# Kernel optimization log

Hardware: AMD Instinct MI355X
Metric: run time of the kernel (lower is better)

The kernel has to match this reference:

```python
import jax, jax.numpy as jnp
import numpy as np

T = 20000          # document length in tokens
EMBED_DIM = 300    # GloVe 840B.300d
STATE_DIM = 400    # 2 * lstm_dim (bidirectional)
HIDDEN = 150       # Scorer hidden_dim default
MAX_N = 10         # span widths 1..10
G_DIM = 2 * STATE_DIM + EMBED_DIM  # 1100


def _mlp3(x, W1, b1, W2, b2, W3, b3):
    # Scorer: Linear -> ReLU -> Linear -> ReLU -> Linear(->1)
    h = jax.nn.relu(x @ W1 + b1)
    h = jax.nn.relu(h @ W2 + b2)
    return h @ W3 + b3


def _span_features(embeds, states, attn_logits):
    """Vectorized SpanEncoder: for every window of width n in 1..MAX_N,
    softmax the per-token attention logits within the window, attention-pool
    the word embeddings, and concat [state_start, state_end, pooled].
    Returns g of shape [sum_n (T-n+1), G_DIM]."""
    gs = []
    for n in range(1, MAX_N + 1):
        S = T - n + 1  # number of width-n spans
        # [n, S] windowed logits and [n, S, E] windowed embeds via shifted slices
        a = jnp.stack([attn_logits[j:j + S] for j in range(n)], axis=0)
        w = jax.nn.softmax(a, axis=0)  # softmax within each span (dim=0 in torch)
        we = jnp.stack([embeds[j:j + S] for j in range(n)], axis=0)
        pooled = jnp.einsum('ns,nse->se', w, we)  # [S, E]
        g = jnp.concatenate([states[:S], states[n - 1:n - 1 + S], pooled], axis=-1)
        gs.append(g)
    return jnp.concatenate(gs, axis=0)


def setup_inputs() -> dict:
    key = jax.random.key(0)
    ks = jax.random.split(key, 16)
    sc = 0.05
    return {
        'embeds': jax.random.normal(ks[0], (T, EMBED_DIM), jnp.float32),
        'states': jax.random.normal(ks[1], (T, STATE_DIM), jnp.float32),
        'attn_W1': jax.random.normal(ks[2], (STATE_DIM, HIDDEN), jnp.float32) * sc,
        'attn_b1': jnp.zeros((HIDDEN,), jnp.float32),
        'attn_W2': jax.random.normal(ks[3], (HIDDEN, HIDDEN), jnp.float32) * sc,
        'attn_b2': jnp.zeros((HIDDEN,), jnp.float32),
        'attn_W3': jax.random.normal(ks[4], (HIDDEN, 1), jnp.float32) * sc,
        'attn_b3': jnp.zeros((1,), jnp.float32),
        'sc_W1': jax.random.normal(ks[5], (G_DIM, HIDDEN), jnp.float32) * sc,
        'sc_b1': jnp.zeros((HIDDEN,), jnp.float32),
        'sc_W2': jax.random.normal(ks[6], (HIDDEN, HIDDEN), jnp.float32) * sc,
        'sc_b2': jnp.zeros((HIDDEN,), jnp.float32),
        'sc_W3': jax.random.normal(ks[7], (HIDDEN, 1), jnp.float32) * sc,
        'sc_b3': jnp.zeros((1,), jnp.float32),
    }


def reference(embeds, states, attn_W1, attn_b1, attn_W2, attn_b2, attn_W3, attn_b3,
              sc_W1, sc_b1, sc_W2, sc_b2, sc_W3, sc_b3):
    # SpanAttention: per-token scalar attention logit from the BiLSTM state
    attn_logits = _mlp3(states, attn_W1, attn_b1, attn_W2, attn_b2, attn_W3, attn_b3)[:, 0]
    # SpanEncoder: ragged windowed attention pooling + boundary-state concat
    g = _span_features(embeds, states, attn_logits)  # [10T-45, 1100]
    # SpanScorer: MLP score per span
    scores = _mlp3(g, sc_W1, sc_b1, sc_W2, sc_b2, sc_W3, sc_b3)[:, 0]
    return scores
```

## Files before the change

kernel.cpp:

```cpp
#include <hip/hip_runtime.h>
#include <hip/hip_bf16.h>
#include <math.h>

#define T_LEN 20000
#define HID 150

typedef __attribute__((ext_vector_type(8))) __bf16 bf16x8;
typedef __attribute__((ext_vector_type(4))) float f32x4;

__device__ __forceinline__ short f2bf(float f) {
    unsigned u = __float_as_uint(f);
    u = (u + 0x7fff + ((u >> 16) & 1)) >> 16;
    return (short)u;
}

__device__ __forceinline__ unsigned pk2(float a, float b) {
    __hip_bfloat162 h = __float22bfloat162_rn(make_float2(a, b));
    return *(unsigned*)&h;
}

__device__ __forceinline__ bf16x8 cvt8(float4 a, float4 b) {
    union { unsigned u[4]; bf16x8 v; } r;
    r.u[0] = pk2(a.x, a.y);
    r.u[1] = pk2(a.z, a.w);
    r.u[2] = pk2(b.x, b.y);
    r.u[3] = pk2(b.z, b.w);
    return r.v;
}

__device__ __forceinline__ float2 ubf2(unsigned u) {
    return make_float2(__uint_as_float(u << 16),
                       __uint_as_float(u & 0xffff0000u));
}

__global__ __launch_bounds__(256) void wprep(
    const float* __restrict__ sc_W1, const float* __restrict__ attn_W1,
    const float* __restrict__ attn_W2, const float* __restrict__ sc_W2,
    short* __restrict__ frag)
{
    int t = blockIdx.x * 256 + threadIdx.x;
    if (t >= 302080) return;
    float v = 0.f;
    if (t < 199680) {
        int e = t & 7, g = t >> 3;
        int lane = g & 63, h = g >> 6;
        int ks = h % 13, nt = h / 13;
        int k = ks * 32 + (lane >> 4) * 8 + e;
        int cs = (nt % 10) * 16 + (lane & 15);
        if (k < 400 && cs < HID) {
            if (nt < 10)      v = sc_W1[(long)k * HID + cs];
            else if (nt < 20) v = sc_W1[(long)(400 + k) * HID + cs];
            else              v = attn_W1[(long)k * HID + cs];
        }
    } else if (t < 250880) {
        int r = t - 199680;
        int e = r & 7, g = r >> 3;
        int lane = g & 63, h = g >> 6;
        int ks = h % 10, nt = h / 10;
        int k = ks * 32 + (lane >> 4) * 8 + e;
        int cs = nt * 16 + (lane & 15);
        if (k < 300 && cs < HID) v = sc_W1[(long)(800 + k) * HID + cs];
    } else if (t < 276480) {
        int r = t - 250880;
        int e = r & 7, g = r >> 3;
        int lane = g & 63, h = g >> 6;
        int ks = h % 5, nt = h / 5;
        int k = ks * 32 + (lane >> 4) * 8 + e;
        int cs = nt * 16 + (lane & 15);
        if (k < HID && cs < HID) v = attn_W2[(long)k * HID + cs];
    } else {
        int r = t - 276480;
        int e = r & 7, g = r >> 3;
        int lane = g & 63, h = g >> 6;
        int ks = h % 5, nt = h / 5;
        int k = ks * 32 + (lane >> 4) * 8 + e;
        int cs = nt * 16 + (lane & 15);
        if (k < HID && cs < HID) v = sc_W2[(long)k * HID + cs];
    }
    frag[t] = f2bf(v);
}

__global__ __launch_bounds__(256) void fusedAP(
    const float* __restrict__ states, const float* __restrict__ embeds,
    const short* __restrict__ frag,
    const float* __restrict__ scb1, const float* __restrict__ ab1,
    const float* __restrict__ ab2, const float* __restrict__ aW3,
    const float* __restrict__ ab3,
    short* __restrict__ Ubf, short* __restrict__ Vbf, short* __restrict__ Pbf,
    float* __restrict__ logits)
{
    __shared__ short As[13 * 64 * 8];
    __shared__ short h1s[16 * 168];
    __shared__ float red[16][4];
    __shared__ float sb1[160], ab1s[160];
    const int tid = threadIdx.x;
    const int w = tid >> 6, lane = tid & 63;
    const int ml = lane & 15, kg = lane >> 4;
    const int m0 = blockIdx.x * 16;

    for (int t = tid; t < 160; t += 256) {
        sb1[t]  = (t < HID) ? scb1[t] : 0.f;
        ab1s[t] = (t < HID) ? ab1[t]  : 0.f;
    }
    for (int g = tid; g < 13 * 64; g += 256) {
        int ks = g >> 6, l2 = g & 63;
        int k = ks * 32 + ((l2 >> 4) << 3);
        const float* Ar = states + (long)(m0 + (l2 & 15)) * 400;
        float4 a0 = make_float4(0.f, 0.f, 0.f, 0.f), a1 = a0;
        if (k + 4 <= 400) a0 = *(const float4*)&Ar[k];
        if (k + 8 <= 400) a1 = *(const float4*)&Ar[k + 4];
        *(bf16x8*)&As[g * 8] = cvt8(a0, a1);
    }
    __syncthreads();

    const short* fb = frag + lane * 8;

    if (blockIdx.y == 0) {
        const int t5 = w * 5;
        f32x4 acc[5];
        #pragma unroll
        for (int t = 0; t < 5; ++t) acc[t] = (f32x4){0.f, 0.f, 0.f, 0.f};

        #pragma unroll
        for (int ks = 0; ks < 13; ++ks) {
            bf16x8 af = *(const bf16x8*)&As[(ks * 64 + lane) * 8];
            bf16x8 bfr[5];
            #pragma unroll
            for (int t = 0; t < 5; ++t)
                bfr[t] = *(const bf16x8*)&fb[((t5 + t) * 13 + ks) << 9];
            #pragma unroll
            for (int t = 0; t < 5; ++t)
                acc[t] = __builtin_amdgcn_mfma_f32_16x16x32_bf16(bfr[t], af, acc[t], 0, 0, 0);
        }

        #pragma unroll
        for (int t = 0; t < 5; ++t) {
            int nt = t5 + t;
            if (w < 2) {
                int col0 = nt * 16 + kg * 4;
                float v[4];
                #pragma unroll
                for (int r = 0; r < 4; ++r) {
                    int c = col0 + r;
                    v[r] = (c < HID) ? acc[t][r] + sb1[c] : 0.f;
                }
                *(uint2*)&Ubf[(long)(m0 + ml) * 160 + col0] =
                    make_uint2(pk2(v[0], v[1]), pk2(v[2], v[3]));
            } else {
                int col0 = (nt - 10) * 16 + kg * 4;
                float v[4];
                #pragma unroll
                for (int r = 0; r < 4; ++r) {
                    int c = col0 + r;
                    v[r] = (c < HID) ? acc[t][r] : 0.f;
                }
                *(uint2*)&Vbf[(long)(m0 + ml) * 160 + col0] =
                    make_uint2(pk2(v[0], v[1]), pk2(v[2], v[3]));
            }
        }
        return;
    }

    const int nT = (w < 2) ? 3 : 2;
    const int t0 = (w < 2) ? 3 * w : 6 + 2 * (w - 2);

    {
        f32x4 acc[3];
        #pragma unroll
        for (int t = 0; t < 3; ++t) acc[t] = (f32x4){0.f, 0.f, 0.f, 0.f};

        #pragma unroll
        for (int ks = 0; ks < 13; ++ks) {
            bf16x8 af = *(const bf16x8*)&As[(ks * 64 + lane) * 8];
            bf16x8 bfr[3];
            #pragma unroll
            for (int t = 0; t < 3; ++t)
                if (t < nT)
                    bfr[t] = *(const bf16x8*)&fb[((20 + t0 + t) * 13 + ks) << 9];
            #pragma unroll
            for (int t = 0; t < 3; ++t)
                if (t < nT)
                    acc[t] = __builtin_amdgcn_mfma_f32_16x16x32_bf16(bfr[t], af, acc[t], 0, 0, 0);
        }

        #pragma unroll
        for (int t = 0; t < 3; ++t) {
            if (t < nT) {
                int col0 = (t0 + t) * 16 + kg * 4;
                float v[4];
                #pragma unroll
                for (int r = 0; r < 4; ++r) {
                    int c = col0 + r;
                    v[r] = (c < HID) ? fmaxf(acc[t][r] + ab1s[c], 0.f) : 0.f;
                }
                *(uint2*)&h1s[ml * 168 + col0] =
                    make_uint2(pk2(v[0], v[1]), pk2(v[2], v[3]));
            }
        }
    }
    __syncthreads();

    for (int g = tid; g < 10 * 64; g += 256) {
        int ks = g >> 6, l2 = g & 63;
        int k = ks * 32 + ((l2 >> 4) << 3);
        const float* Er = embeds + (long)(m0 + (l2 & 15)) * 300;
        float4 a0 = make_float4(0.f, 0.f, 0.f, 0.f), a1 = a0;
        if (k + 4 <= 300) a0 = *(const float4*)&Er[k];
        if (k + 8 <= 300) a1 = *(const float4*)&Er[k + 4];
        *(bf16x8*)&As[g * 8] = cvt8(a0, a1);
    }

    {
        const short* fAt2 = frag + 250880 + lane * 8;
        bf16x8 af2[5];
        #pragma unroll
        for (int ks = 0; ks < 5; ++ks)
            af2[ks] = *(const bf16x8*)&h1s[ml * 168 + ks * 32 + kg * 8];

        float score[4] = {0.f, 0.f, 0.f, 0.f};
        #pragma unroll
        for (int t = 0; t < 3; ++t) {
            if (t < nT) {
                int nt = t0 + t;
                bf16x8 wb[5];
                #pragma unroll
                for (int ks = 0; ks < 5; ++ks)
                    wb[ks] = *(const bf16x8*)&fAt2[(nt * 5 + ks) << 9];
                f32x4 a2 = {0.f, 0.f, 0.f, 0.f};
                #pragma unroll
                for (int ks = 0; ks < 5; ++ks)
                    a2 = __builtin_amdgcn_mfma_f32_16x16x32_bf16(af2[ks], wb[ks], a2, 0, 0, 0);
                int col = nt * 16 + ml;
                float b2v = (col < HID) ? ab2[col] : 0.f;
                float w3v = (col < HID) ? aW3[col] : 0.f;
                #pragma unroll
                for (int r = 0; r < 4; ++r)
                    score[r] += fmaxf(a2[r] + b2v, 0.f) * w3v;
            }
        }
        #pragma unroll
        for (int r = 0; r < 4; ++r) {
            score[r] += __shfl_xor(score[r], 1);
            score[r] += __shfl_xor(score[r], 2);
            score[r] += __shfl_xor(score[r], 4);
            score[r] += __shfl_xor(score[r], 8);
        }
        if (ml == 0) {
            #pragma unroll
            for (int r = 0; r < 4; ++r) red[kg * 4 + r][w] = score[r];
        }
    }
    __syncthreads();

    {
        const short* fP = frag + 199680 + lane * 8;
        f32x4 accP[3];
        #pragma unroll
        for (int t = 0; t < 3; ++t) accP[t] = (f32x4){0.f, 0.f, 0.f, 0.f};

        #pragma unroll
        for (int ks = 0; ks < 10; ++ks) {
            bf16x8 af = *(const bf16x8*)&As[(ks * 64 + lane) * 8];
            bf16x8 bfr[3];
            #pragma unroll
            for (int t = 0; t < 3; ++t)
                if (t < nT)
                    bfr[t] = *(const bf16x8*)&fP[((t0 + t) * 10 + ks) << 9];
            #pragma unroll
            for (int t = 0; t < 3; ++t)
                if (t < nT)
                    accP[t] = __builtin_amdgcn_mfma_f32_16x16x32_bf16(bfr[t], af, accP[t], 0, 0, 0);
        }

        #pragma unroll
        for (int t = 0; t < 3; ++t) {
            if (t < nT) {
                int col0 = (t0 + t) * 16 + kg * 4;
                float v[4];
                #pragma unroll
                for (int r = 0; r < 4; ++r) {
                    int c = col0 + r;
                    v[r] = (c < HID) ? accP[t][r] : 0.f;
                }
                *(uint2*)&Pbf[(long)(m0 + ml) * 160 + col0] =
                    make_uint2(pk2(v[0], v[1]), pk2(v[2], v[3]));
            }
        }
    }

    if (tid < 16)
        logits[m0 + tid] = red[tid][0] + red[tid][1] + red[tid][2] + red[tid][3] + ab3[0];
}

__global__ __launch_bounds__(256) void span_all(
    const short* __restrict__ Ubf, const short* __restrict__ Vbf,
    const short* __restrict__ Pbf, const float* __restrict__ logits,
    const short* __restrict__ fW2, const float* __restrict__ b2,
    const float* __restrict__ W3, const float* __restrict__ b3,
    float* __restrict__ out)
{
    __shared__ short h1s[2][32 * 168];
    __shared__ float red[2][32][2];
    __shared__ float Ls[48], ebuf[48];
    __shared__ float b2s[160], W3s[160];

    const int tid = threadIdx.x;
    const int s0 = blockIdx.x * 32;
    const int nlo = 2 * blockIdx.y + 1;
    const int nhi = nlo + 1;

    if (tid < 48) {
        int r = s0 + tid; if (r > T_LEN - 1) r = T_LEN - 1;
        Ls[tid] = (tid < 41) ? logits[r] : -1e30f;
    }
    for (int t = tid; t < 160; t += 256) {
        b2s[t] = (t < HID) ? b2[t] : 0.f;
        W3s[t] = (t < HID) ? W3[t] : 0.f;
    }
    __syncthreads();
    if (tid < 48) {
        float M = -1e30f;
        for (int t = 0; t < 41; ++t) M = fmaxf(M, Ls[t]);
        ebuf[tid] = (tid < 41) ? expf(Ls[tid] - M) : 0.f;
    }
    __syncthreads();

    const int i = tid >> 3;
    const int q = tid & 7;
    const int d0 = 20 * q;
    const int s = s0 + i;
    int su = s; if (su > T_LEN - 1) su = T_LEN - 1;

    float Ur[20];
    {
        const uint2* U2 = (const uint2*)&Ubf[(long)su * 160 + d0];
        #pragma unroll
        for (int c = 0; c < 5; ++c) {
            uint2 uv = U2[c];
            float2 a = ubf2(uv.x), b_ = ubf2(uv.y);
            Ur[4 * c + 0] = a.x;  Ur[4 * c + 1] = a.y;
            Ur[4 * c + 2] = b_.x; Ur[4 * c + 3] = b_.y;
        }
    }
    float accp[20];
    #pragma unroll
    for (int d = 0; d < 20; ++d) accp[d] = 0.f;
    float den = 0.f;

    for (int j = 0; j < nlo - 1; ++j) {
        int rr_ = s + j; if (rr_ > T_LEN - 1) rr_ = T_LEN - 1;
        float e = ebuf[i + j];
        den += e;
        const uint2* P2 = (const uint2*)&Pbf[(long)rr_ * 160 + d0];
        #pragma unroll
        for (int c = 0; c < 5; ++c) {
            uint2 pv = P2[c];
            float2 a = ubf2(pv.x), b_ = ubf2(pv.y);
            accp[4 * c + 0] += e * a.x;  accp[4 * c + 1] += e * a.y;
            accp[4 * c + 2] += e * b_.x; accp[4 * c + 3] += e * b_.y;
        }
    }

    const int w = tid >> 6, lane = tid & 63;
    const int ml = lane & 15, kg = lane >> 4;
    const int mt = w >> 1;
    const int nt0 = (w & 1) * 5;
    const float bb = b3[0];

    auto phase1 = [&](int n, int p) {
        int rr_ = s + n - 1; if (rr_ > T_LEN - 1) rr_ = T_LEN - 1;
        float e = ebuf[i + n - 1];
        den += e;
        {
            const uint2* P2 = (const uint2*)&Pbf[(long)rr_ * 160 + d0];
            #pragma unroll
            for (int c = 0; c < 5; ++c) {
                uint2 pv = P2[c];
                float2 a = ubf2(pv.x), b_ = ubf2(pv.y);
                accp[4 * c + 0] += e * a.x;  accp[4 * c + 1] += e * a.y;
                accp[4 * c + 2] += e * b_.x; accp[4 * c + 3] += e * b_.y;
            }
        }
        float invd = 1.f / den;
        {
            const uint2* V2 = (const uint2*)&Vbf[(long)rr_ * 160 + d0];
            #pragma unroll
            for (int c = 0; c < 5; ++c) {
                uint2 vv = V2[c];
                float2 a = ubf2(vv.x), b_ = ubf2(vv.y);
                float x0 = fmaxf(Ur[4 * c + 0] + a.x  + accp[4 * c + 0] * invd, 0.f);
                float x1 = fmaxf(Ur[4 * c + 1] + a.y  + accp[4 * c + 1] * invd, 0.f);
                float x2 = fmaxf(Ur[4 * c + 2] + b_.x + accp[4 * c + 2] * invd, 0.f);
                float x3 = fmaxf(Ur[4 * c + 3] + b_.y + accp[4 * c + 3] * invd, 0.f);
                *(uint2*)&h1s[p][i * 168 + d0 + 4 * c] =
                    make_uint2(pk2(x0, x1), pk2(x2, x3));
            }
        }
    };

    phase1(nlo, 0);
    __syncthreads();

    for (int n = nlo; n <= nhi; ++n) {
        const int p = (n - nlo) & 1;
        if (n < nhi) phase1(n + 1, 1 - p);

        bf16x8 af[5];
        #pragma unroll
        for (int ks = 0; ks < 5; ++ks)
            af[ks] = *(const bf16x8*)&h1s[p][(mt * 16 + ml) * 168 + ks * 32 + kg * 8];

        float sc[4] = {0.f, 0.f, 0.f, 0.f};
        #pragma unroll
        for (int j = 0; j < 5; ++j) {
            int nt = nt0 + j;
            f32x4 a2 = {0.f, 0.f, 0.f, 0.f};
            #pragma unroll
            for (int ks = 0; ks < 5; ++ks) {
                bf16x8 bf = *(const bf16x8*)&fW2[(long)(((nt * 5 + ks) << 6) | lane) << 3];
                a2 = __builtin_amdgcn_mfma_f32_16x16x32_bf16(af[ks], bf, a2, 0, 0, 0);
            }
            int col = nt * 16 + ml;
            float b2v = b2s[col], w3v = W3s[col];
            #pragma unroll
            for (int r = 0; r < 4; ++r)
                sc[r] += fmaxf(a2[r] + b2v, 0.f) * w3v;
        }
        #pragma unroll
        for (int r = 0; r < 4; ++r) {
            sc[r] += __shfl_xor(sc[r], 1);
            sc[r] += __shfl_xor(sc[r], 2);
            sc[r] += __shfl_xor(sc[r], 4);
            sc[r] += __shfl_xor(sc[r], 8);
        }
        if (ml == 0) {
            #pragma unroll
            for (int r = 0; r < 4; ++r)
                red[p][mt * 16 + kg * 4 + r][w & 1] = sc[r];
        }
        __syncthreads();
        if (tid < 32) {
            int S = T_LEN - n + 1;
            int off = (n - 1) * (T_LEN + 1) - (n - 1) * n / 2;
            int sr = s0 + tid;
            if (sr < S) out[off + sr] = red[p][tid][0] + red[p][tid][1] + bb;
        }
    }
}

extern "C" void kernel_launch(void* const* d_in, const int* in_sizes, int n_in,
                              void* d_out, int out_size, void* d_ws, size_t ws_size,
                              hipStream_t stream) {
    const float* embeds  = (const float*)d_in[0];
    const float* states  = (const float*)d_in[1];
    const float* attn_W1 = (const float*)d_in[2];
    const float* attn_b1 = (const float*)d_in[3];
    const float* attn_W2 = (const float*)d_in[4];
    const float* attn_b2 = (const float*)d_in[5];
    const float* attn_W3 = (const float*)d_in[6];
    const float* attn_b3 = (const float*)d_in[7];
    const float* sc_W1   = (const float*)d_in[8];
    const float* sc_b1   = (const float*)d_in[9];
    const float* sc_W2   = (const float*)d_in[10];
    const float* sc_b2   = (const float*)d_in[11];
    const float* sc_W3   = (const float*)d_in[12];
    const float* sc_b3   = (const float*)d_in[13];
    float* out = (float*)d_out;

    short* wsS = (short*)d_ws;
    short* Ubf = wsS;
    short* Vbf = wsS + 3200256;
    short* Pbf = wsS + 6400512;
    short* frag = wsS + 9600768;
    float* logits = (float*)(wsS + 9902848);

    wprep<<<1180, 256, 0, stream>>>(sc_W1, attn_W1, attn_W2, sc_W2, frag);
    fusedAP<<<dim3(1250, 2), 256, 0, stream>>>(states, embeds, frag, sc_b1, attn_b1,
                                               attn_b2, attn_W3, attn_b3,
                                               Ubf, Vbf, Pbf, logits);
    span_all<<<dim3(625, 5), 256, 0, stream>>>(Ubf, Vbf, Pbf, logits,
                                               frag + 276480, sc_b2, sc_W3, sc_b3,
                                               out);
}
```

Measured before the change: 203.2 us.

## Make projection kernel persistent with register-resident weights and prefetched input tiles

The per-token projection kernel becomes a persistent 512-thread grid of 250x3 blocks. Each block keeps its weight fragments in registers and loops over 16-row chunks, prefetching the next chunk's states or embeds into registers while the MFMAs on the current chunk run. Work is split three ways (U/V, V plus attention MLP, P projection) so weights are not reloaded from global memory for every tile. The span kernel is regrouped from five pairs of widths per block to two groups of five widths, which raises per-block work but cuts grid size. The cost is higher register pressure and fewer blocks in flight.

```diff
diff --git a/kernel.cpp b/kernel.cpp
--- a/kernel.cpp
+++ b/kernel.cpp
@@ -80,7 +80,22 @@
     frag[t] = f2bf(v);
 }
 
-__global__ __launch_bounds__(256) void fusedAP(
+template<int KS, int K>
+__device__ __forceinline__ void stage_sync(const float* __restrict__ src,
+                                           int m0, int tid, short* As)
+{
+    for (int idx = tid; idx < KS * 64; idx += 512) {
+        int ks = idx >> 6, l2 = idx & 63;
+        int k = ks * 32 + ((l2 >> 4) << 3);
+        const float* Ar = src + (long)(m0 + (l2 & 15)) * K;
+        float4 a0 = make_float4(0.f, 0.f, 0.f, 0.f), a1 = a0;
+        if (k + 4 <= K) a0 = *(const float4*)&Ar[k];
+        if (k + 8 <= K) a1 = *(const float4*)&Ar[k + 4];
+        *(bf16x8*)&As[idx * 8] = cvt8(a0, a1);
+    }
+}
+
+__global__ __launch_bounds__(512) void fusedT(
     const float* __restrict__ states, const float* __restrict__ embeds,
     const short* __restrict__ frag,
     const float* __restrict__ scb1, const float* __restrict__ ab1,
@@ -91,205 +106,287 @@
 {
     __shared__ short As[13 * 64 * 8];
     __shared__ short h1s[16 * 168];
-    __shared__ float red[16][4];
+    __shared__ float red[16][8];
     __shared__ float sb1[160], ab1s[160];
+
     const int tid = threadIdx.x;
     const int w = tid >> 6, lane = tid & 63;
     const int ml = lane & 15, kg = lane >> 4;
-    const int m0 = blockIdx.x * 16;
-
-    for (int t = tid; t < 160; t += 256) {
+
+    for (int t = tid; t < 160; t += 512) {
         sb1[t]  = (t < HID) ? scb1[t] : 0.f;
         ab1s[t] = (t < HID) ? ab1[t]  : 0.f;
     }
-    for (int g = tid; g < 13 * 64; g += 256) {
-        int ks = g >> 6, l2 = g & 63;
-        int k = ks * 32 + ((l2 >> 4) << 3);
-        const float* Ar = states + (long)(m0 + (l2 & 15)) * 400;
-        float4 a0 = make_float4(0.f, 0.f, 0.f, 0.f), a1 = a0;
-        if (k + 4 <= 400) a0 = *(const float4*)&Ar[k];
-        if (k + 8 <= 400) a1 = *(const float4*)&Ar[k + 4];
-        *(bf16x8*)&As[g * 8] = cvt8(a0, a1);
-    }
-    __syncthreads();
-
-    const short* fb = frag + lane * 8;
 
     if (blockIdx.y == 0) {
-        const int t5 = w * 5;
-        f32x4 acc[5];
-        #pragma unroll
-        for (int t = 0; t < 5; ++t) acc[t] = (f32x4){0.f, 0.f, 0.f, 0.f};
-
-        #pragma unroll
-        for (int ks = 0; ks < 13; ++ks) {
-            bf16x8 af = *(const bf16x8*)&As[(ks * 64 + lane) * 8];
-            bf16x8 bfr[5];
-            #pragma unroll
-            for (int t = 0; t < 5; ++t)
-                bfr[t] = *(const bf16x8*)&fb[((t5 + t) * 13 + ks) << 9];
-            #pragma unroll
-            for (int t = 0; t < 5; ++t)
-                acc[t] = __builtin_amdgcn_mfma_f32_16x16x32_bf16(bfr[t], af, acc[t], 0, 0, 0);
-        }
-
-        #pragma unroll
-        for (int t = 0; t < 5; ++t) {
-            int nt = t5 + t;
-            if (w < 2) {
-                int col0 = nt * 16 + kg * 4;
-                float v[4];
+        const int t0 = 2 * w;
+        bf16x8 wA[2][13];
+        #pragma unroll
+        for (int t = 0; t < 2; ++t)
+            #pragma unroll
+            for (int ks = 0; ks < 13; ++ks)
+                wA[t][ks] = *(const bf16x8*)&frag[(((t0 + t) * 13 + ks) << 9) + lane * 8];
+
+        int c = blockIdx.x;
+        stage_sync<13, 400>(states, c * 16, tid, As);
+        __syncthreads();
+
+        for (; c < 1250; c += 250) {
+            const int cn = c + 250;
+            float4 qa[2][2];
+            #pragma unroll
+            for (int it = 0; it < 2; ++it) {
+                int idx = tid + (it << 9);
+                if (cn < 1250 && idx < 832) {
+                    int ks = idx >> 6, l2 = idx & 63;
+                    int k = ks * 32 + ((l2 >> 4) << 3);
+                    const float* Ar = states + (long)(cn * 16 + (l2 & 15)) * 400;
+                    qa[it][0] = (k + 4 <= 400) ? *(const float4*)&Ar[k]     : make_float4(0.f,0.f,0.f,0.f);
+                    qa[it][1] = (k + 8 <= 400) ? *(const float4*)&Ar[k + 4] : make_float4(0.f,0.f,0.f,0.f);
+                }
+            }
+
+            const int m0 = c * 16;
+            f32x4 acc[2];
+            acc[0] = (f32x4){0.f, 0.f, 0.f, 0.f};
+            acc[1] = (f32x4){0.f, 0.f, 0.f, 0.f};
+            #pragma unroll
+            for (int ks = 0; ks < 13; ++ks) {
+                bf16x8 af = *(const bf16x8*)&As[(ks * 64 + lane) * 8];
+                acc[0] = __builtin_amdgcn_mfma_f32_16x16x32_bf16(wA[0][ks], af, acc[0], 0, 0, 0);
+                acc[1] = __builtin_amdgcn_mfma_f32_16x16x32_bf16(wA[1][ks], af, acc[1], 0, 0, 0);
+            }
+            #pragma unroll
+            for (int t = 0; t < 2; ++t) {
+                int nt = t0 + t;
+                if (nt < 10) {
+                    int col0 = nt * 16 + kg * 4;
+                    float v[4];
+                    #pragma unroll
+                    for (int r = 0; r < 4; ++r) {
+                        int cc = col0 + r;
+                        v[r] = (cc < HID) ? acc[t][r] + sb1[cc] : 0.f;
+                    }
+                    *(uint2*)&Ubf[(long)(m0 + ml) * 160 + col0] =
+                        make_uint2(pk2(v[0], v[1]), pk2(v[2], v[3]));
+                } else {
+                    int col0 = (nt - 10) * 16 + kg * 4;
+                    float v[4];
+                    #pragma unroll
+                    for (int r = 0; r < 4; ++r) {
+                        int cc = col0 + r;
+                        v[r] = (cc < HID) ? acc[t][r] : 0.f;
+                    }
+                    *(uint2*)&Vbf[(long)(m0 + ml) * 160 + col0] =
+                        make_uint2(pk2(v[0], v[1]), pk2(v[2], v[3]));
+                }
+            }
+            __syncthreads();
+            if (cn < 1250) {
+                #pragma unroll
+                for (int it = 0; it < 2; ++it) {
+                    int idx = tid + (it << 9);
+                    if (idx < 832) *(bf16x8*)&As[idx * 8] = cvt8(qa[it][0], qa[it][1]);
+                }
+            }
+            __syncthreads();
+        }
+    } else if (blockIdx.y == 1) {
+        const int nTi = (w < 6) ? 2 : 1;
+        const int t0 = (w < 6) ? 16 + 2 * w : 28 + (w - 6);
+        bf16x8 wA[2][13];
+        #pragma unroll
+        for (int t = 0; t < 2; ++t)
+            if (t < nTi) {
+                #pragma unroll
+                for (int ks = 0; ks < 13; ++ks)
+                    wA[t][ks] = *(const bf16x8*)&frag[(((t0 + t) * 13 + ks) << 9) + lane * 8];
+            }
+        const int ct0 = (w < 2) ? 2 * w : w + 2;
+        const int nC = (w < 2) ? 2 : 1;
+        const short* fAt2 = frag + 250880 + lane * 8;
+
+        int c = blockIdx.x;
+        stage_sync<13, 400>(states, c * 16, tid, As);
+        __syncthreads();
+
+        for (; c < 1250; c += 250) {
+            const int cn = c + 250;
+            float4 qa[2][2];
+            #pragma unroll
+            for (int it = 0; it < 2; ++it) {
+                int idx = tid + (it << 9);
+                if (cn < 1250 && idx < 832) {
+                    int ks = idx >> 6, l2 = idx & 63;
+                    int k = ks * 32 + ((l2 >> 4) << 3);
+                    const float* Ar = states + (long)(cn * 16 + (l2 & 15)) * 400;
+                    qa[it][0] = (k + 4 <= 400) ? *(const float4*)&Ar[k]     : make_float4(0.f,0.f,0.f,0.f);
+                    qa[it][1] = (k + 8 <= 400) ? *(const float4*)&Ar[k + 4] : make_float4(0.f,0.f,0.f,0.f);
+                }
+            }
+
+            const int m0 = c * 16;
+            f32x4 acc[2];
+            acc[0] = (f32x4){0.f, 0.f, 0.f, 0.f};
+            acc[1] = (f32x4){0.f, 0.f, 0.f, 0.f};
+            #pragma unroll
+            for (int ks = 0; ks < 13; ++ks) {
+                bf16x8 af = *(const bf16x8*)&As[(ks * 64 + lane) * 8];
+                #pragma unroll
+                for (int t = 0; t < 2; ++t)
+                    if (t < nTi)
+                        acc[t] = __builtin_amdgcn_mfma_f32_16x16x32_bf16(wA[t][ks], af, acc[t], 0, 0, 0);
+            }
+            #pragma unroll
+            for (int t = 0; t < 2; ++t) {
+                if (t < nTi) {
+                    int nt = t0 + t;
+                    if (nt < 20) {
+                        int col0 = (nt - 10) * 16 + kg * 4;
+                        float v[4];
+                        #pragma unroll
+                        for (int r = 0; r < 4; ++r) {
+                            int cc = col0 + r;
+                            v[r] = (cc < HID) ? acc[t][r] : 0.f;
+                        }
+                        *(uint2*)&Vbf[(long)(m0 + ml) * 160 + col0] =
+                            make_uint2(pk2(v[0], v[1]), pk2(v[2], v[3]));
+                    } else {
+                        int col0 = (nt - 20) * 16 + kg * 4;
+                        float v[4];
+                        #pragma unroll
+                        for (int r = 0; r < 4; ++r) {
+                            int cc = col0 + r;
+                            v[r] = (cc < HID) ? fmaxf(acc[t][r] + ab1s[cc], 0.f) : 0.f;
+                        }
+                        *(uint2*)&h1s[ml * 168 + col0] =
+                            make_uint2(pk2(v[0], v[1]), pk2(v[2], v[3]));
+                    }
+                }
+            }
+            __syncthreads();
+
+            {
+                bf16x8 af2[5];
+                #pragma unroll
+                for (int ks = 0; ks < 5; ++ks)
+                    af2[ks] = *(const bf16x8*)&h1s[ml * 168 + ks * 32 + kg * 8];
+
+                float score[4] = {0.f, 0.f, 0.f, 0.f};
+                #pragma unroll
+                for (int t = 0; t < 2; ++t) {
+                    if (t < nC) {
+                        int nt = ct0 + t;
+                        bf16x8 wb[5];
+                        #pragma unroll
+                        for (int ks = 0; ks < 5; ++ks)
+                            wb[ks] = *(const bf16x8*)&fAt2[(nt * 5 + ks) << 9];
+                        f32x4 a2 = {0.f, 0.f, 0.f, 0.f};
+                        #pragma unroll
+                        for (int ks = 0; ks < 5; ++ks)
+                            a2 = __builtin_amdgcn_mfma_f32_16x16x32_bf16(af2[ks], wb[ks], a2, 0, 0, 0);
+                        int col = nt * 16 + ml;
+                        float b2v = (col < HID) ? ab2[col] : 0.f;
+                        float w3v = (col < HID) ? aW3[col] : 0.f;
+                        #pragma unroll
+                        for (int r = 0; r < 4; ++r)
+                            score[r] += fmaxf(a2[r] + b2v, 0.f) * w3v;
+                    }
+                }
                 #pragma unroll
                 for (int r = 0; r < 4; ++r) {
-                    int c = col0 + r;
-                    v[r] = (c < HID) ? acc[t][r] + sb1[c] : 0.f;
-                }
-                *(uint2*)&Ubf[(long)(m0 + ml) * 160 + col0] =
-                    make_uint2(pk2(v[0], v[1]), pk2(v[2], v[3]));
-            } else {
-                int col0 = (nt - 10) * 16 + kg * 4;
-                float v[4];
-                #pragma unroll
-                for (int r = 0; r < 4; ++r) {
-                    int c = col0 + r;
-                    v[r] = (c < HID) ? acc[t][r] : 0.f;
-                }
-                *(uint2*)&Vbf[(long)(m0 + ml) * 160 + col0] =
-                    make_uint2(pk2(v[0], v[1]), pk2(v[2], v[3]));
-            }
-        }
-        return;
-    }
-
-    const int nT = (w < 2) ? 3 : 2;
-    const int t0 = (w < 2) ? 3 * w : 6 + 2 * (w - 2);
-
-    {
-        f32x4 acc[3];
-        #pragma unroll
-        for (int t = 0; t < 3; ++t) acc[t] = (f32x4){0.f, 0.f, 0.f, 0.f};
-
-        #pragma unroll
-        for (int ks = 0; ks < 13; ++ks) {
-            bf16x8 af = *(const bf16x8*)&As[(ks * 64 + lane) * 8];
-            bf16x8 bfr[3];
-            #pragma unroll
-            for (int t = 0; t < 3; ++t)
-                if (t < nT)
-                    bfr[t] = *(const bf16x8*)&fb[((20 + t0 + t) * 13 + ks) << 9];
-            #pragma unroll
-            for (int t = 0; t < 3; ++t)
-                if (t < nT)
-                    acc[t] = __builtin_amdgcn_mfma_f32_16x16x32_bf16(bfr[t], af, acc[t], 0, 0, 0);
-        }
-
-        #pragma unroll
-        for (int t = 0; t < 3; ++t) {
-            if (t < nT) {
-                int col0 = (t0 + t) * 16 + kg * 4;
-                float v[4];
-                #pragma unroll
-                for (int r = 0; r < 4; ++r) {
-                    int c = col0 + r;
-                    v[r] = (c < HID) ? fmaxf(acc[t][r] + ab1s[c], 0.f) : 0.f;
-                }
-                *(uint2*)&h1s[ml * 168 + col0] =
-                    make_uint2(pk2(v[0], v[1]), pk2(v[2], v[3]));
-            }
-        }
-    }
-    __syncthreads();
-
-    for (int g = tid; g < 10 * 64; g += 256) {
-        int ks = g >> 6, l2 = g & 63;
-        int k = ks * 32 + ((l2 >> 4) << 3);
-        const float* Er = embeds + (long)(m0 + (l2 & 15)) * 300;
-        float4 a0 = make_float4(0.f, 0.f, 0.f, 0.f), a1 = a0;
-        if (k + 4 <= 300) a0 = *(const float4*)&Er[k];
-        if (k + 8 <= 300) a1 = *(const float4*)&Er[k + 4];
-        *(bf16x8*)&As[g * 8] = cvt8(a0, a1);
-    }
-
-    {
-        const short* fAt2 = frag + 250880 + lane * 8;
-        bf16x8 af2[5];
-        #pragma unroll
-        for (int ks = 0; ks < 5; ++ks)
-            af2[ks] = *(const bf16x8*)&h1s[ml * 168 + ks * 32 + kg * 8];
-
-        float score[4] = {0.f, 0.f, 0.f, 0.f};
-        #pragma unroll
-        for (int t = 0; t < 3; ++t) {
-            if (t < nT) {
-                int nt = t0 + t;
-                bf16x8 wb[5];
-                #pragma unroll
-                for (int ks = 0; ks < 5; ++ks)
-                    wb[ks] = *(const bf16x8*)&fAt2[(nt * 5 + ks) << 9];
-                f32x4 a2 = {0.f, 0.f, 0.f, 0.f};
-                #pragma unroll
-                for (int ks = 0; ks < 5; ++ks)
-                    a2 = __builtin_amdgcn_mfma_f32_16x16x32_bf16(af2[ks], wb[ks], a2, 0, 0, 0);
-                int col = nt * 16 + ml;
-                float b2v = (col < HID) ? ab2[col] : 0.f;
-                float w3v = (col < HID) ? aW3[col] : 0.f;
-                #pragma unroll
-                for (int r = 0; r < 4; ++r)
-                    score[r] += fmaxf(a2[r] + b2v, 0.f) * w3v;
-            }
-        }
-        #pragma unroll
-        for (int r = 0; r < 4; ++r) {
-            score[r] += __shfl_xor(score[r], 1);
-            score[r] += __shfl_xor(score[r], 2);
-            score[r] += __shfl_xor(score[r], 4);
-            score[r] += __shfl_xor(score[r], 8);
-        }
-        if (ml == 0) {
-            #pragma unroll
-            for (int r = 0; r < 4; ++r) red[kg * 4 + r][w] = score[r];
-        }
-    }
-    __syncthreads();
-
-    {
-        const short* fP = frag + 199680 + lane * 8;
-        f32x4 accP[3];
-        #pragma unroll
-        for (int t = 0; t < 3; ++t) accP[t] = (f32x4){0.f, 0.f, 0.f, 0.f};
-
-        #pragma unroll
-        for (int ks = 0; ks < 10; ++ks) {
-            bf16x8 af = *(const bf16x8*)&As[(ks * 64 + lane) * 8];
-            bf16x8 bfr[3];
-            #pragma unroll
-            for (int t = 0; t < 3; ++t)
-                if (t < nT)
-                    bfr[t] = *(const bf16x8*)&fP[((t0 + t) * 10 + ks) << 9];
-            #pragma unroll
-            for (int t = 0; t < 3; ++t)
-                if (t < nT)
-                    accP[t] = __builtin_amdgcn_mfma_f32_16x16x32_bf16(bfr[t], af, accP[t], 0, 0, 0);
-        }
-
-        #pragma unroll
-        for (int t = 0; t < 3; ++t) {
-            if (t < nT) {
-                int col0 = (t0 + t) * 16 + kg * 4;
-                float v[4];
-                #pragma unroll
-                for (int r = 0; r < 4; ++r) {
-                    int c = col0 + r;
-                    v[r] = (c < HID) ? accP[t][r] : 0.f;
-                }
-                *(uint2*)&Pbf[(long)(m0 + ml) * 160 + col0] =
-                    make_uint2(pk2(v[0], v[1]), pk2(v[2], v[3]));
-            }
-        }
-    }
-
-    if (tid < 16)
-        logits[m0 + tid] = red[tid][0] + red[tid][1] + red[tid][2] + red[tid][3] + ab3[0];
+                    score[r] += __shfl_xor(score[r], 1);
+                    score[r] += __shfl_xor(score[r], 2);
+                    score[r] += __shfl_xor(score[r], 4);
+                    score[r] += __shfl_xor(score[r], 8);
+                }
+                if (ml == 0) {
+                    #pragma unroll
+                    for (int r = 0; r < 4; ++r) red[kg * 4 + r][w] = score[r];
+                }
+            }
+            __syncthreads();
+            if (tid < 16)
+                logits[m0 + tid] = red[tid][0] + red[tid][1] + red[tid][2] + red[tid][3] +
+                                   red[tid][4] + red[tid][5] + red[tid][6] + red[tid][7] + ab3[0];
+
+            if (cn < 1250) {
+                #pragma unroll
+                for (int it = 0; it < 2; ++it) {
+                    int idx = tid + (it << 9);
+                    if (idx < 832) *(bf16x8*)&As[idx * 8] = cvt8(qa[it][0], qa[it][1]);
+                }
+            }
+            __syncthreads();
+        }
+    } else {
+        const int nP = (w < 2) ? 2 : 1;
+        const int t0 = (w < 2) ? 2 * w : w + 2;
+        bf16x8 wP[2][10];
+        #pragma unroll
+        for (int t = 0; t < 2; ++t)
+            if (t < nP) {
+                #pragma unroll
+                for (int ks = 0; ks < 10; ++ks)
+                    wP[t][ks] = *(const bf16x8*)&frag[199680 + (((t0 + t) * 10 + ks) << 9) + lane * 8];
+            }
+
+        int c = blockIdx.x;
+        stage_sync<10, 300>(embeds, c * 16, tid, As);
+        __syncthreads();
+
+        for (; c < 1250; c += 250) {
+            const int cn = c + 250;
+            float4 qa[2][2];
+            #pragma unroll
+            for (int it = 0; it < 2; ++it) {
+                int idx = tid + (it << 9);
+                if (cn < 1250 && idx < 640) {
+                    int ks = idx >> 6, l2 = idx & 63;
+                    int k = ks * 32 + ((l2 >> 4) << 3);
+                    const float* Ar = embeds + (long)(cn * 16 + (l2 & 15)) * 300;
+                    qa[it][0] = (k + 4 <= 300) ? *(const float4*)&Ar[k]     : make_float4(0.f,0.f,0.f,0.f);
+                    qa[it][1] = (k + 8 <= 300) ? *(const float4*)&Ar[k + 4] : make_float4(0.f,0.f,0.f,0.f);
+                }
+            }
+
+            const int m0 = c * 16;
+            f32x4 acc[2];
+            acc[0] = (f32x4){0.f, 0.f, 0.f, 0.f};
+            acc[1] = (f32x4){0.f, 0.f, 0.f, 0.f};
+            #pragma unroll
+            for (int ks = 0; ks < 10; ++ks) {
+                bf16x8 af = *(const bf16x8*)&As[(ks * 64 + lane) * 8];
+                #pragma unroll
+                for (int t = 0; t < 2; ++t)
+                    if (t < nP)
+                        acc[t] = __builtin_amdgcn_mfma_f32_16x16x32_bf16(wP[t][ks], af, acc[t], 0, 0, 0);
+            }
+            #pragma unroll
+            for (int t = 0; t < 2; ++t) {
+                if (t < nP) {
+                    int col0 = (t0 + t) * 16 + kg * 4;
+                    float v[4];
+                    #pragma unroll
+                    for (int r = 0; r < 4; ++r) {
+                        int cc = col0 + r;
+                        v[r] = (cc < HID) ? acc[t][r] : 0.f;
+                    }
+                    *(uint2*)&Pbf[(long)(m0 + ml) * 160 + col0] =
+                        make_uint2(pk2(v[0], v[1]), pk2(v[2], v[3]));
+                }
+            }
+            __syncthreads();
+            if (cn < 1250) {
+                #pragma unroll
+                for (int it = 0; it < 2; ++it) {
+                    int idx = tid + (it << 9);
+                    if (idx < 640) *(bf16x8*)&As[idx * 8] = cvt8(qa[it][0], qa[it][1]);
+                }
+            }
+            __syncthreads();
+        }
+    }
 }
 
 __global__ __launch_bounds__(256) void span_all(
@@ -306,8 +403,8 @@
 
     const int tid = threadIdx.x;
     const int s0 = blockIdx.x * 32;
-    const int nlo = 2 * blockIdx.y + 1;
-    const int nhi = nlo + 1;
+    const int nlo = blockIdx.y ? 6 : 1;
+    const int nhi = blockIdx.y ? 10 : 5;
 
     if (tid < 48) {
         int r = s0 + tid; if (r > T_LEN - 1) r = T_LEN - 1;
@@ -475,10 +572,10 @@
     float* logits = (float*)(wsS + 9902848);
 
     wprep<<<1180, 256, 0, stream>>>(sc_W1, attn_W1, attn_W2, sc_W2, frag);
-    fusedAP<<<dim3(1250, 2), 256, 0, stream>>>(states, embeds, frag, sc_b1, attn_b1,
-                                               attn_b2, attn_W3, attn_b3,
-                                               Ubf, Vbf, Pbf, logits);
-    span_all<<<dim3(625, 5), 256, 0, stream>>>(Ubf, Vbf, Pbf, logits,
+    fusedT<<<dim3(250, 3), 512, 0, stream>>>(states, embeds, frag, sc_b1, attn_b1,
+                                             attn_b2, attn_W3, attn_b3,
+                                             Ubf, Vbf, Pbf, logits);
+    span_all<<<dim3(625, 2), 256, 0, stream>>>(Ubf, Vbf, Pbf, logits,
                                                frag + 276480, sc_b2, sc_W3, sc_b3,
                                                out);
 }
```

Result: faster. 185.4 us (-8.8%).
